# Kernel tuning notes

Measured on AMD Instinct MI355X. Metric: run time of the kernel, lower is better.

Reference implementation:

```python
import jax, jax.numpy as jnp
import numpy as np

B, IN, H, OUT = 8192, 1024, 1024, 512


def setup_inputs() -> dict:
    key = jax.random.key(0)
    ks = jax.random.split(key, 13)
    s_in = 1.0 / np.sqrt(IN + H)
    s_h = 1.0 / np.sqrt(H)
    return {
        "x": jax.random.normal(ks[0], (B, IN), jnp.float32),
        "h": jax.random.normal(ks[1], (B, H), jnp.float32),
        "c": jax.random.normal(ks[2], (B, H), jnp.float32),
        "Wi": jax.random.normal(ks[3], (IN + H, H), jnp.float32) * s_in,
        "bi": jax.random.normal(ks[4], (H,), jnp.float32) * s_in,
        "Wf": jax.random.normal(ks[5], (IN + H, H), jnp.float32) * s_in,
        "bf": jax.random.normal(ks[6], (H,), jnp.float32) * s_in,
        "Wo": jax.random.normal(ks[7], (IN + H, H), jnp.float32) * s_in,
        "bo": jax.random.normal(ks[8], (H,), jnp.float32) * s_in,
        "Wc": jax.random.normal(ks[9], (IN + H, H), jnp.float32) * s_in,
        "bc": jax.random.normal(ks[10], (H,), jnp.float32) * s_in,
        "Wy": jax.random.normal(ks[11], (H, OUT), jnp.float32) * s_h,
        "by": jax.random.normal(ks[12], (OUT,), jnp.float32) * s_h,
    }


def reference(x, h, c, Wi, bi, Wf, bf, Wo, bo, Wc, bc, Wy, by):
    # combined: [B, IN+H]
    combined = jnp.concatenate([x, h], axis=1)
    # Fuse the four gate matmuls into one [B, IN+H] x [IN+H, 4H] GEMM.
    W_all = jnp.concatenate([Wi, Wf, Wo, Wc], axis=1)        # [IN+H, 4H]
    b_all = jnp.concatenate([bi, bf, bo, bc], axis=0)        # [4H]
    gates = combined @ W_all + b_all                          # [B, 4H]
    gi, gf, go, gc = jnp.split(gates, 4, axis=1)
    i_t = jax.nn.sigmoid(gi)
    f_t = jax.nn.sigmoid(gf)
    o_t = jax.nn.sigmoid(go)
    c_tilde = jnp.tanh(gc)
    c_new = f_t * c + i_t * c_tilde
    h_new = o_t * jnp.tanh(c_new)
    y_hat = h_new @ Wy + by                                   # [B, OUT]
    return (y_hat, (h_new, c_new))
```

## Files before the change

kernel.cpp:

```cpp
#include <hip/hip_runtime.h>
#include <hip/hip_bf16.h>
#include <stdint.h>

#define B_ 8192
#define IN_ 1024
#define H_ 1024
#define OUT_ 512
#define KC 2048
#define N4 4096

typedef __bf16 bf16_t;
typedef __bf16 bf16x8 __attribute__((ext_vector_type(8)));
typedef float f32x4 __attribute__((ext_vector_type(4)));

__device__ __forceinline__ void gload_lds16(const void* g, void* l) {
  __builtin_amdgcn_global_load_lds(
      (const __attribute__((address_space(1))) uint32_t*)g,
      (__attribute__((address_space(3))) uint32_t*)l, 16, 0, 0);
}

__device__ __forceinline__ float fsigmoid(float x) {
  return __builtin_amdgcn_rcpf(1.0f + __expf(-x));
}
__device__ __forceinline__ float ftanh(float x) {
  return 2.0f * __builtin_amdgcn_rcpf(1.0f + __expf(-2.0f * x)) - 1.0f;
}


__global__ __launch_bounds__(256) void pack_combined(
    const float* __restrict__ x, const float* __restrict__ h,
    bf16_t* __restrict__ out) {
  const int row = blockIdx.x;
  const int j = threadIdx.x * 8;
  const float* src = (j < IN_) ? (x + (size_t)row * IN_ + j)
                               : (h + (size_t)row * H_ + (j - IN_));
  float4 a = ((const float4*)src)[0];
  float4 b = ((const float4*)src)[1];
  bf16x8 v;
  v[0] = (bf16_t)a.x; v[1] = (bf16_t)a.y; v[2] = (bf16_t)a.z; v[3] = (bf16_t)a.w;
  v[4] = (bf16_t)b.x; v[5] = (bf16_t)b.y; v[6] = (bf16_t)b.z; v[7] = (bf16_t)b.w;
  *(bf16x8*)(out + (size_t)row * KC + j) = v;
}

__global__ __launch_bounds__(256) void transpose_pack(
    const float* __restrict__ src, bf16_t* __restrict__ dst, int K, int N) {
  __shared__ float tile[64][65];
  const int k0 = blockIdx.y * 64, n0 = blockIdx.x * 64;
  const int t = threadIdx.x;
  const int tr = t >> 4, tc4 = (t & 15) * 4;
#pragma unroll
  for (int r = 0; r < 4; ++r) {
    const int k = tr + r * 16;
    float4 v = *(const float4*)(src + (size_t)(k0 + k) * N + n0 + tc4);
    tile[k][tc4] = v.x; tile[k][tc4 + 1] = v.y;
    tile[k][tc4 + 2] = v.z; tile[k][tc4 + 3] = v.w;
  }
  __syncthreads();
  const int nr = t >> 3, kc8 = (t & 7) * 8;
#pragma unroll
  for (int r = 0; r < 2; ++r) {
    const int n = nr + r * 32;
    bf16x8 v;
#pragma unroll
    for (int q = 0; q < 8; ++q) v[q] = (bf16_t)tile[kc8 + q][n];
    *(bf16x8*)(dst + (size_t)(n0 + n) * K + k0 + kc8) = v;
  }
}

__global__ __launch_bounds__(512) void gemm1_8ph(
    const bf16_t* __restrict__ A, const bf16_t* __restrict__ Bt,
    bf16_t* __restrict__ C) {
  constexpr int K = KC, N = N4;
  constexpr int NT = K / 64;
  __shared__ char lds[131072];

  const int tid = threadIdx.x;
  const int lane = tid & 63;
  const int w = tid >> 6;
  const int wr = w >> 2, wc = w & 3;
  const int l15 = lane & 15, l4 = lane >> 4;

  const int wg = blockIdx.x;
  const int swz = (wg & 7) * 64 + (wg >> 3);
  const int bx = swz >> 5;
  const int by = swz & 31;
  const int m0 = by * 256, n0 = bx * 256;

  const int jrow = lane >> 2;
  const int jcol = ((lane & 3) * 16) ^ ((lane >> 5) << 5);
  const char* Asrc = (const char*)A + (size_t)(m0 + w * 16 + jrow) * (K * 2) + jcol;
  const char* Bsrc = (const char*)Bt + (size_t)(n0 + w * 16 + jrow) * (K * 2) + jcol;
  char* ldsA = lds;
  char* ldsB = lds + 32768;
  const int wchunk = w * 2048;

#define STG_A(buf, h, tt) do {                                            \
    gload_lds16(Asrc + (size_t)(h) * 128 * (K * 2) + (size_t)(tt) * 128,  \
                ldsA + (buf) * 65536 + (h) * 16384 + wchunk);             \
    gload_lds16(Asrc + (size_t)(h) * 128 * (K * 2) + (size_t)(tt) * 128 + 64, \
                ldsA + (buf) * 65536 + (h) * 16384 + wchunk + 1024);      \
  } while (0)
#define STG_B(buf, h, tt) do {                                            \
    gload_lds16(Bsrc + (size_t)(h) * 128 * (K * 2) + (size_t)(tt) * 128,  \
                ldsB + (buf) * 65536 + (h) * 16384 + wchunk);             \
    gload_lds16(Bsrc + (size_t)(h) * 128 * (K * 2) + (size_t)(tt) * 128 + 64, \
                ldsB + (buf) * 65536 + (h) * 16384 + wchunk + 1024);      \
  } while (0)

  const int rdoff = l15 * 64 + ((l4 * 16) ^ ((l15 >> 3) << 5));
  const char* ldsArd = lds + wr * 16384 + rdoff;
  const char* ldsBrd = lds + 32768 + (wc >> 1) * 16384 + (wc & 1) * 8192 + rdoff;

  f32x4 acc[8][4] = {};
  bf16x8 fa[4][2], fb[4][2];

#define MFMA_Q(MIBASE, NIBASE)                                                \
  do {                                                                        \
    __builtin_amdgcn_s_setprio(1);                                            \
    _Pragma("unroll") for (int mi = 0; mi < 4; ++mi)                          \
        _Pragma("unroll") for (int ni = 0; ni < 2; ++ni)                      \
            _Pragma("unroll") for (int kk = 0; kk < 2; ++kk)                  \
                acc[(MIBASE) + mi][(NIBASE) + ni] =                           \
                    __builtin_amdgcn_mfma_f32_16x16x32_bf16(                  \
                        fa[mi][kk], fb[(NIBASE) + ni][kk],                    \
                        acc[(MIBASE) + mi][(NIBASE) + ni], 0, 0, 0);          \
    __builtin_amdgcn_s_setprio(0);                                            \
  } while (0)

  STG_B(0, 0, 0); STG_A(0, 0, 0); STG_A(0, 1, 0); STG_B(0, 1, 0);
  STG_B(1, 0, 1); STG_A(1, 0, 1); STG_A(1, 1, 1);
  asm volatile("s_waitcnt vmcnt(6)" ::: "memory");
  __builtin_amdgcn_s_barrier();

  for (int t = 0; t < NT; ++t) {
    const int buf = t & 1;
    const int nbuf = buf ^ 1;
    const char* ard = ldsArd + buf * 65536;
    const char* brd = ldsBrd + buf * 65536;
    const bool st1 = (t + 1 < NT);
    const bool st2 = (t + 2 < NT);

#pragma unroll
    for (int mi = 0; mi < 4; ++mi)
#pragma unroll
      for (int kk = 0; kk < 2; ++kk)
        fa[mi][kk] = *(const bf16x8*)(ard + mi * 2048 + kk * 1024);
#pragma unroll
    for (int ni = 0; ni < 2; ++ni)
#pragma unroll
      for (int kk = 0; kk < 2; ++kk)
        fb[ni][kk] = *(const bf16x8*)(brd + ni * 2048 + kk * 1024);
    if (st1) STG_B(nbuf, 1, t + 1);
    __builtin_amdgcn_s_barrier();
    MFMA_Q(0, 0);
    __builtin_amdgcn_s_barrier();

#pragma unroll
    for (int ni = 2; ni < 4; ++ni)
#pragma unroll
      for (int kk = 0; kk < 2; ++kk)
        fb[ni][kk] = *(const bf16x8*)(brd + ni * 2048 + kk * 1024);
    __builtin_amdgcn_s_barrier();
    MFMA_Q(0, 2);
    __builtin_amdgcn_s_barrier();

#pragma unroll
    for (int mi = 0; mi < 4; ++mi)
#pragma unroll
      for (int kk = 0; kk < 2; ++kk)
        fa[mi][kk] = *(const bf16x8*)(ard + (mi + 4) * 2048 + kk * 1024);
    if (st2) STG_B(buf, 0, t + 2);
    __builtin_amdgcn_s_barrier();
    MFMA_Q(4, 0);
    __builtin_amdgcn_s_barrier();

    if (st2) { STG_A(buf, 0, t + 2); STG_A(buf, 1, t + 2); }
    __builtin_amdgcn_s_barrier();
    MFMA_Q(4, 2);
    if (st2) asm volatile("s_waitcnt vmcnt(6)" ::: "memory");
    else     asm volatile("s_waitcnt vmcnt(0)" ::: "memory");
    __builtin_amdgcn_s_barrier();
  }

  const int col0 = n0 + wc * 64 + l15;
  const int row0 = m0 + wr * 128 + l4 * 4;
#pragma unroll
  for (int mi = 0; mi < 8; ++mi)
#pragma unroll
    for (int ni = 0; ni < 4; ++ni)
#pragma unroll
      for (int q = 0; q < 4; ++q)
        C[(size_t)(row0 + mi * 16 + q) * N + col0 + ni * 16] =
            (bf16_t)acc[mi][ni][q];
#undef STG_A
#undef STG_B
#undef MFMA_Q
}

__global__ __launch_bounds__(256) void gemm_bt_f32(
    const bf16_t* __restrict__ A, const bf16_t* __restrict__ Bt,
    float* __restrict__ Cout, const float* __restrict__ bias,
    int M, int N, int K) {
  __shared__ bf16_t As[128 * 64];
  __shared__ bf16_t Bs[128 * 64];
  const int tid = threadIdx.x;
  const int lane = tid & 63;
  const int wave = tid >> 6;
  const int m0 = blockIdx.y * 128;
  const int n0 = blockIdx.x * 128;
  const int wr = wave >> 1, wc = wave & 1;
  const int l15 = lane & 15, l4 = lane >> 4;

  f32x4 acc[4][4] = {};

  const int srow = tid >> 3;
  const int skel = (tid & 7) * 8;
  const size_t aBase = (size_t)(m0 + srow) * K + skel;
  const size_t bBase = (size_t)(n0 + srow) * K + skel;
  char* aL = (char*)As + wave * 1024;
  char* bL = (char*)Bs + wave * 1024;

  for (int kt = 0; kt < K; kt += 64) {
    __syncthreads();
#pragma unroll
    for (int i = 0; i < 4; ++i) {
      gload_lds16(A + aBase + (size_t)i * 32 * K + kt, aL + i * 4096);
      gload_lds16(Bt + bBase + (size_t)i * 32 * K + kt, bL + i * 4096);
    }
    __syncthreads();
#pragma unroll
    for (int kk = 0; kk < 2; ++kk) {
      bf16x8 af[4], bq[4];
#pragma unroll
      for (int mi = 0; mi < 4; ++mi)
        af[mi] = *(const bf16x8*)((const char*)As +
                 (wr * 64 + mi * 16 + l15) * 128 + kk * 64 + l4 * 16);
#pragma unroll
      for (int ni = 0; ni < 4; ++ni)
        bq[ni] = *(const bf16x8*)((const char*)Bs +
                 (wc * 64 + ni * 16 + l15) * 128 + kk * 64 + l4 * 16);
#pragma unroll
      for (int mi = 0; mi < 4; ++mi)
#pragma unroll
        for (int ni = 0; ni < 4; ++ni)
          acc[mi][ni] = __builtin_amdgcn_mfma_f32_16x16x32_bf16(
              af[mi], bq[ni], acc[mi][ni], 0, 0, 0);
    }
  }

  const int col = n0 + wc * 64 + l15;
  const int row0 = m0 + wr * 64 + l4 * 4;
#pragma unroll
  for (int ni = 0; ni < 4; ++ni) {
    const float bv = bias[col + ni * 16];
#pragma unroll
    for (int mi = 0; mi < 4; ++mi)
#pragma unroll
      for (int q = 0; q < 4; ++q)
        Cout[(size_t)(row0 + mi * 16 + q) * N + col + ni * 16] =
            acc[mi][ni][q] + bv;
  }
}

__global__ __launch_bounds__(256) void lstm_eltwise(
    const bf16_t* __restrict__ gates, const float* __restrict__ c,
    const float* __restrict__ bi, const float* __restrict__ bfg,
    const float* __restrict__ bo, const float* __restrict__ bc,
    float* __restrict__ h_out, float* __restrict__ c_out,
    bf16_t* __restrict__ hb) {
  const int idx = blockIdx.x * 256 + threadIdx.x;
  const int row = idx >> 7;
  const int j = (idx & 127) * 8;
  const size_t gbase = (size_t)row * N4 + j;
  bf16x8 gi = *(const bf16x8*)(gates + gbase);
  bf16x8 gf = *(const bf16x8*)(gates + gbase + H_);
  bf16x8 go = *(const bf16x8*)(gates + gbase + 2 * H_);
  bf16x8 gc = *(const bf16x8*)(gates + gbase + 3 * H_);
  const size_t cbase = (size_t)row * H_ + j;
  float4 c0 = *(const float4*)(c + cbase);
  float4 c1 = *(const float4*)(c + cbase + 4);
  float cv[8] = {c0.x, c0.y, c0.z, c0.w, c1.x, c1.y, c1.z, c1.w};
  float hnew[8], cnew[8];
  bf16x8 hbv;
#pragma unroll
  for (int q = 0; q < 8; ++q) {
    float I = fsigmoid((float)gi[q] + bi[j + q]);
    float F = fsigmoid((float)gf[q] + bfg[j + q]);
    float O = fsigmoid((float)go[q] + bo[j + q]);
    float Ct = ftanh((float)gc[q] + bc[j + q]);
    float cn = F * cv[q] + I * Ct;
    cnew[q] = cn;
    float hn = O * ftanh(cn);
    hnew[q] = hn;
    hbv[q] = (bf16_t)hn;
  }
  *(float4*)(c_out + cbase) = make_float4(cnew[0], cnew[1], cnew[2], cnew[3]);
  *(float4*)(c_out + cbase + 4) = make_float4(cnew[4], cnew[5], cnew[6], cnew[7]);
  *(float4*)(h_out + cbase) = make_float4(hnew[0], hnew[1], hnew[2], hnew[3]);
  *(float4*)(h_out + cbase + 4) = make_float4(hnew[4], hnew[5], hnew[6], hnew[7]);
  *(bf16x8*)(hb + cbase) = hbv;
}

extern "C" void kernel_launch(void* const* d_in, const int* in_sizes, int n_in,
                              void* d_out, int out_size, void* d_ws,
                              size_t ws_size, hipStream_t stream) {
  const float* x = (const float*)d_in[0];
  const float* h = (const float*)d_in[1];
  const float* c = (const float*)d_in[2];
  const float* Wi = (const float*)d_in[3];
  const float* bi = (const float*)d_in[4];
  const float* Wf = (const float*)d_in[5];
  const float* bfg = (const float*)d_in[6];
  const float* Wo = (const float*)d_in[7];
  const float* bo = (const float*)d_in[8];
  const float* Wc = (const float*)d_in[9];
  const float* bc = (const float*)d_in[10];
  const float* Wy = (const float*)d_in[11];
  const float* by = (const float*)d_in[12];

  char* ws = (char*)d_ws;
  bf16_t* combined = (bf16_t*)ws;
  bf16_t* Wt = (bf16_t*)(ws + 33554432);
  bf16_t* Wyt = (bf16_t*)(ws + 33554432 + 16777216);
  bf16_t* gates = (bf16_t*)(ws + 33554432 + 16777216 + 1048576);
  bf16_t* hb = (bf16_t*)(ws + 33554432 + 16777216 + 1048576 + 67108864);

  float* y_out = (float*)d_out;
  float* h_out = y_out + (size_t)B_ * OUT_;
  float* c_out = h_out + (size_t)B_ * H_;

  pack_combined<<<dim3(B_), dim3(256), 0, stream>>>(x, h, combined);
  const float* Wg[4] = {Wi, Wf, Wo, Wc};
  for (int g = 0; g < 4; ++g)
    transpose_pack<<<dim3(H_ / 64, KC / 64), dim3(256), 0, stream>>>(
        Wg[g], Wt + (size_t)g * H_ * KC, KC, H_);
  transpose_pack<<<dim3(OUT_ / 64, H_ / 64), dim3(256), 0, stream>>>(
      Wy, Wyt, H_, OUT_);

  gemm1_8ph<<<dim3((B_ / 256) * (N4 / 256)), dim3(512), 0, stream>>>(
      combined, Wt, gates);

  lstm_eltwise<<<dim3(B_ * H_ / 8 / 256), dim3(256), 0, stream>>>(
      gates, c, bi, bfg, bo, bc, h_out, c_out, hb);

  gemm_bt_f32<<<dim3(OUT_ / 128, B_ / 128), dim3(256), 0, stream>>>(
      hb, Wyt, y_out, by, B_, OUT_, H_);
}
```

Before: 226.8 us.

## Fuse LSTM elementwise into gate GEMM epilogue via interleaved gate weight layout

Gate weight columns are interleaved so that each 256-wide GEMM tile holds the i/f/o/c gates for the same 64 hidden units. The GEMM epilogue stages the fp32 accumulators through swizzled LDS and computes the LSTM cell update directly, writing h, c and bf16 h. This removes the separate elementwise kernel and the 64 MB bf16 gates round-trip through global memory. It also keeps gates in fp32 before the activations, and it reorders the MFMA loop nest. The epilogue stores are scalar 4-byte writes, and it adds extra barriers.

```diff
diff --git a/kernel.cpp b/kernel.cpp
--- a/kernel.cpp
+++ b/kernel.cpp
@@ -43,7 +43,8 @@
 }
 
 __global__ __launch_bounds__(256) void transpose_pack(
-    const float* __restrict__ src, bf16_t* __restrict__ dst, int K, int N) {
+    const float* __restrict__ src, bf16_t* __restrict__ dst, int K, int N,
+    int RS, int RO) {
   __shared__ float tile[64][65];
   const int k0 = blockIdx.y * 64, n0 = blockIdx.x * 64;
   const int t = threadIdx.x;
@@ -63,14 +64,18 @@
     bf16x8 v;
 #pragma unroll
     for (int q = 0; q < 8; ++q) v[q] = (bf16_t)tile[kc8 + q][n];
-    *(bf16x8*)(dst + (size_t)(n0 + n) * K + k0 + kc8) = v;
+    *(bf16x8*)(dst + (size_t)((n0 + n) * RS + RO) * K + k0 + kc8) = v;
   }
 }
 
 __global__ __launch_bounds__(512) void gemm1_8ph(
     const bf16_t* __restrict__ A, const bf16_t* __restrict__ Bt,
-    bf16_t* __restrict__ C) {
-  constexpr int K = KC, N = N4;
+    const float* __restrict__ c_in,
+    const float* __restrict__ bi, const float* __restrict__ bfg,
+    const float* __restrict__ bo, const float* __restrict__ bc,
+    float* __restrict__ h_out, float* __restrict__ c_out,
+    bf16_t* __restrict__ hb) {
+  constexpr int K = KC;
   constexpr int NT = K / 64;
   __shared__ char lds[131072];
 
@@ -117,9 +122,9 @@
 #define MFMA_Q(MIBASE, NIBASE)                                                \
   do {                                                                        \
     __builtin_amdgcn_s_setprio(1);                                            \
-    _Pragma("unroll") for (int mi = 0; mi < 4; ++mi)                          \
-        _Pragma("unroll") for (int ni = 0; ni < 2; ++ni)                      \
-            _Pragma("unroll") for (int kk = 0; kk < 2; ++kk)                  \
+    _Pragma("unroll") for (int kk = 0; kk < 2; ++kk)                          \
+        _Pragma("unroll") for (int mi = 0; mi < 4; ++mi)                      \
+            _Pragma("unroll") for (int ni = 0; ni < 2; ++ni)                  \
                 acc[(MIBASE) + mi][(NIBASE) + ni] =                           \
                     __builtin_amdgcn_mfma_f32_16x16x32_bf16(                  \
                         fa[mi][kk], fb[(NIBASE) + ni][kk],                    \
@@ -182,16 +187,49 @@
     __builtin_amdgcn_s_barrier();
   }
 
-  const int col0 = n0 + wc * 64 + l15;
-  const int row0 = m0 + wr * 128 + l4 * 4;
-#pragma unroll
-  for (int mi = 0; mi < 8; ++mi)
-#pragma unroll
-    for (int ni = 0; ni < 4; ++ni)
-#pragma unroll
-      for (int q = 0; q < 4; ++q)
-        C[(size_t)(row0 + mi * 16 + q) * N + col0 + ni * 16] =
-            (bf16_t)acc[mi][ni][q];
+  const int hc0 = n0 >> 2;
+  float* ldsF = (float*)lds;
+  const int ehc = tid & 63;
+  const int err0 = (tid >> 6) * 8;
+  const float bI = bi[hc0 + ehc];
+  const float bF = bfg[hc0 + ehc];
+  const float bO = bo[hc0 + ehc];
+  const float bC = bc[hc0 + ehc];
+
+  for (int ch = 0; ch < 4; ++ch) {
+    __builtin_amdgcn_s_barrier();
+    if (wr == (ch >> 1)) {
+      const int mib = (ch & 1) * 4;
+#pragma unroll
+      for (int mi = 0; mi < 4; ++mi)
+#pragma unroll
+        for (int ni = 0; ni < 4; ++ni) {
+          const int col = wc * 64 + ni * 16 + l15;
+          const int hc = col >> 2, g = col & 3;
+#pragma unroll
+          for (int q = 0; q < 4; ++q) {
+            const int rr = mi * 16 + l4 * 4 + q;
+            ldsF[rr * 256 + ((hc ^ rr) * 4) + g] = acc[mib + mi][ni][q];
+          }
+        }
+    }
+    __builtin_amdgcn_s_barrier();
+#pragma unroll
+    for (int r = 0; r < 8; ++r) {
+      const int rr = err0 + r;
+      f32x4 gq = *(const f32x4*)&ldsF[rr * 256 + ((ehc ^ rr) * 4)];
+      const size_t gidx = (size_t)(m0 + ch * 64 + rr) * H_ + hc0 + ehc;
+      float I = fsigmoid(gq[0] + bI);
+      float F = fsigmoid(gq[1] + bF);
+      float O = fsigmoid(gq[2] + bO);
+      float Ct = ftanh(gq[3] + bC);
+      float cn = F * c_in[gidx] + I * Ct;
+      float hn = O * ftanh(cn);
+      c_out[gidx] = cn;
+      h_out[gidx] = hn;
+      hb[gidx] = (bf16_t)hn;
+    }
+  }
 #undef STG_A
 #undef STG_B
 #undef MFMA_Q
@@ -260,45 +298,6 @@
         Cout[(size_t)(row0 + mi * 16 + q) * N + col + ni * 16] =
             acc[mi][ni][q] + bv;
   }
-}
-
-__global__ __launch_bounds__(256) void lstm_eltwise(
-    const bf16_t* __restrict__ gates, const float* __restrict__ c,
-    const float* __restrict__ bi, const float* __restrict__ bfg,
-    const float* __restrict__ bo, const float* __restrict__ bc,
-    float* __restrict__ h_out, float* __restrict__ c_out,
-    bf16_t* __restrict__ hb) {
-  const int idx = blockIdx.x * 256 + threadIdx.x;
-  const int row = idx >> 7;
-  const int j = (idx & 127) * 8;
-  const size_t gbase = (size_t)row * N4 + j;
-  bf16x8 gi = *(const bf16x8*)(gates + gbase);
-  bf16x8 gf = *(const bf16x8*)(gates + gbase + H_);
-  bf16x8 go = *(const bf16x8*)(gates + gbase + 2 * H_);
-  bf16x8 gc = *(const bf16x8*)(gates + gbase + 3 * H_);
-  const size_t cbase = (size_t)row * H_ + j;
-  float4 c0 = *(const float4*)(c + cbase);
-  float4 c1 = *(const float4*)(c + cbase + 4);
-  float cv[8] = {c0.x, c0.y, c0.z, c0.w, c1.x, c1.y, c1.z, c1.w};
-  float hnew[8], cnew[8];
-  bf16x8 hbv;
-#pragma unroll
-  for (int q = 0; q < 8; ++q) {
-    float I = fsigmoid((float)gi[q] + bi[j + q]);
-    float F = fsigmoid((float)gf[q] + bfg[j + q]);
-    float O = fsigmoid((float)go[q] + bo[j + q]);
-    float Ct = ftanh((float)gc[q] + bc[j + q]);
-    float cn = F * cv[q] + I * Ct;
-    cnew[q] = cn;
-    float hn = O * ftanh(cn);
-    hnew[q] = hn;
-    hbv[q] = (bf16_t)hn;
-  }
-  *(float4*)(c_out + cbase) = make_float4(cnew[0], cnew[1], cnew[2], cnew[3]);
-  *(float4*)(c_out + cbase + 4) = make_float4(cnew[4], cnew[5], cnew[6], cnew[7]);
-  *(float4*)(h_out + cbase) = make_float4(hnew[0], hnew[1], hnew[2], hnew[3]);
-  *(float4*)(h_out + cbase + 4) = make_float4(hnew[4], hnew[5], hnew[6], hnew[7]);
-  *(bf16x8*)(hb + cbase) = hbv;
 }
 
 extern "C" void kernel_launch(void* const* d_in, const int* in_sizes, int n_in,
@@ -322,8 +321,7 @@
   bf16_t* combined = (bf16_t*)ws;
   bf16_t* Wt = (bf16_t*)(ws + 33554432);
   bf16_t* Wyt = (bf16_t*)(ws + 33554432 + 16777216);
-  bf16_t* gates = (bf16_t*)(ws + 33554432 + 16777216 + 1048576);
-  bf16_t* hb = (bf16_t*)(ws + 33554432 + 16777216 + 1048576 + 67108864);
+  bf16_t* hb = (bf16_t*)(ws + 33554432 + 16777216 + 1048576);
 
   float* y_out = (float*)d_out;
   float* h_out = y_out + (size_t)B_ * OUT_;
@@ -333,15 +331,12 @@
   const float* Wg[4] = {Wi, Wf, Wo, Wc};
   for (int g = 0; g < 4; ++g)
     transpose_pack<<<dim3(H_ / 64, KC / 64), dim3(256), 0, stream>>>(
-        Wg[g], Wt + (size_t)g * H_ * KC, KC, H_);
+        Wg[g], Wt, KC, H_, 4, g);
   transpose_pack<<<dim3(OUT_ / 64, H_ / 64), dim3(256), 0, stream>>>(
-      Wy, Wyt, H_, OUT_);
+      Wy, Wyt, H_, OUT_, 1, 0);
 
   gemm1_8ph<<<dim3((B_ / 256) * (N4 / 256)), dim3(512), 0, stream>>>(
-      combined, Wt, gates);
-
-  lstm_eltwise<<<dim3(B_ * H_ / 8 / 256), dim3(256), 0, stream>>>(
-      gates, c, bi, bfg, bo, bc, h_out, c_out, hb);
+      combined, Wt, c, bi, bfg, bo, bc, h_out, c_out, hb);
 
   gemm_bt_f32<<<dim3(OUT_ / 128, B_ / 128), dim3(256), 0, stream>>>(
       hb, Wyt, y_out, by, B_, OUT_, H_);
```

Result: faster. 212.2 us (-6.5%).
